# Kernel optimization log

Hardware: AMD Instinct MI355X
Metric: run time of the kernel (lower is better)

Reference implementation:

```python
import jax, jax.numpy as jnp
import numpy as np

D_MODEL = 1024
NUM_HEADS = 16
HEAD_DIM = D_MODEL // NUM_HEADS
B, S = 4, 2048


def setup_inputs() -> dict:
    key = jax.random.key(0)
    ks = jax.random.split(key, 11)
    sc = 1.0 / np.sqrt(D_MODEL)
    return {
        "query": jax.random.normal(ks[0], (B, S, D_MODEL), jnp.float32),
        "key": jax.random.normal(ks[1], (B, S, D_MODEL), jnp.float32),
        "value": jax.random.normal(ks[2], (B, S, D_MODEL), jnp.float32),
        "Wq": jax.random.normal(ks[3], (D_MODEL, D_MODEL), jnp.float32) * sc,
        "bq": jnp.zeros((D_MODEL,), jnp.float32),
        "Wk": jax.random.normal(ks[4], (D_MODEL, D_MODEL), jnp.float32) * sc,
        "bk": jnp.zeros((D_MODEL,), jnp.float32),
        "Wv": jax.random.normal(ks[5], (D_MODEL, D_MODEL), jnp.float32) * sc,
        "bv": jnp.zeros((D_MODEL,), jnp.float32),
        "Wo": jax.random.normal(ks[6], (D_MODEL, D_MODEL), jnp.float32) * sc,
        "bo": jnp.zeros((D_MODEL,), jnp.float32),
    }


def _split_heads(x):
    b, s, _ = x.shape
    return x.reshape(b, s, NUM_HEADS, HEAD_DIM).transpose(0, 2, 1, 3)  # [B,H,S,Dh]


def reference(query, key, value, Wq, bq, Wk, bk, Wv, bv, Wo, bo):
    q = _split_heads(query @ Wq + bq)
    k = _split_heads(key @ Wk + bk)
    v = _split_heads(value @ Wv + bv)
    scores = jnp.einsum("bhqd,bhkd->bhqk", q, k) / np.sqrt(HEAD_DIM)
    attn = jax.nn.softmax(scores, axis=-1)
    out = jnp.einsum("bhqk,bhkd->bhqd", attn, v)
    out = out.transpose(0, 2, 1, 3).reshape(query.shape[0], -1, D_MODEL)
    return out @ Wo + bo
```

## Files before the change

### kernel.cpp

```cpp
#include <hip/hip_runtime.h>

typedef unsigned short u16;
typedef unsigned int   u32;
typedef unsigned long long u64;
typedef __attribute__((ext_vector_type(8))) short bf16x8;
typedef __attribute__((ext_vector_type(4))) float f32x4;

#define S_  2048
#define DH  64
#define DM  1024
#define BS  8192
#define CS  0.18033688011112042f

static __device__ __forceinline__ float bf2f(u16 v){ return __uint_as_float(((u32)v)<<16); }
static __device__ __forceinline__ u16 f2bf(float f){
  u32 x = __float_as_uint(f);
  return (u16)((x + 0x7fffu + ((x>>16)&1u)) >> 16);
}
#if __has_builtin(__builtin_amdgcn_cvt_pk_bf16_f32)
static __device__ __forceinline__ u32 pk2(float x, float y){
  typedef __attribute__((ext_vector_type(2))) __bf16 bf2v;
  union { bf2v v; u32 u; } c; c.v = __builtin_amdgcn_cvt_pk_bf16_f32(x, y); return c.u;
}
#else
static __device__ __forceinline__ u32 pk2(float x, float y){
  return (u32)f2bf(x) | ((u32)f2bf(y) << 16);
}
#endif
#if __has_builtin(__builtin_amdgcn_exp2f)
#define EXP2F(x) __builtin_amdgcn_exp2f(x)
#else
#define EXP2F(x) exp2f(x)
#endif

static __device__ __forceinline__ void dma16(const u16* g, const u16* l){
  __builtin_amdgcn_global_load_lds(
      (const __attribute__((address_space(1))) u32*)(u64)(uintptr_t)g,
      (__attribute__((address_space(3))) u32*)(u32)(u64)(uintptr_t)l, 16, 0, 0);
}

static __device__ __forceinline__ bf16x8 lds_frag(const u16* p){
  union { bf16x8 f; uint2 u[2]; } w;
  w.u[0] = *(const uint2*)(p);
  w.u[1] = *(const uint2*)(p+4);
  return w.f;
}
static __device__ __forceinline__ bf16x8 frag16v(const u16* p){
  union { bf16x8 f; uint4 u; } w;
  w.u = *(const uint4*)p;
  return w.f;
}
static __device__ __forceinline__ void stage16_bf(const u16* __restrict__ g, u16* s){
  uint4 a = *(const uint4*)g;
  uint4 b = *(const uint4*)(g+8);
  *(uint2*)(s+0)  = make_uint2(a.x,a.y);
  *(uint2*)(s+4)  = make_uint2(a.z,a.w);
  *(uint2*)(s+8)  = make_uint2(b.x,b.y);
  *(uint2*)(s+12) = make_uint2(b.z,b.w);
}
static __device__ __forceinline__ void stage16_f32(const float* __restrict__ g, u16* s){
  float4 a0 = ((const float4*)g)[0];
  float4 a1 = ((const float4*)g)[1];
  float4 a2 = ((const float4*)g)[2];
  float4 a3 = ((const float4*)g)[3];
  *(uint2*)(s+0)  = make_uint2(pk2(a0.x,a0.y), pk2(a0.z,a0.w));
  *(uint2*)(s+4)  = make_uint2(pk2(a1.x,a1.y), pk2(a1.z,a1.w));
  *(uint2*)(s+8)  = make_uint2(pk2(a2.x,a2.y), pk2(a2.z,a2.w));
  *(uint2*)(s+12) = make_uint2(pk2(a3.x,a3.y), pk2(a3.z,a3.w));
}

__global__ __launch_bounds__(256) void prep(
    const void* __restrict__ w0, const void* __restrict__ w1,
    const void* __restrict__ w2, const void* __restrict__ w3,
    u16* t0, u16* t1, u16* t2, u16* t3,
    const void* __restrict__ a0, const void* __restrict__ a1,
    const void* __restrict__ a2,
    u16* c0, u16* c1, u16* c2, const int f32f){
  __shared__ u16 tile[32][33];
  int z = blockIdx.z;
  int tid = threadIdx.x;
  bool f32 = f32f != 0;
  if (z < 4){
    const void* in = z==0?w0 : z==1?w1 : z==2?w2 : w3;
    u16* out = z==0?t0 : z==1?t1 : z==2?t2 : t3;
    int tx = tid & 31, ty = tid >> 5;
    int c  = blockIdx.x*32 + tx;
    int r0 = blockIdx.y*32;
    for (int i=ty;i<32;i+=8){
      long off = (long)(r0+i)*DM + c;
      tile[i][tx] = f32 ? f2bf(((const float*)in)[off]) : ((const u16*)in)[off];
    }
    __syncthreads();
    int rr = r0 + tx, cb = blockIdx.x*32;
    for (int i=ty;i<32;i+=8) out[(long)(cb+i)*DM + rr] = tile[tx][i];
  } else {
    if (!f32) return;
    const void* in = z==4?a0 : z==5?a1 : a2;
    u16* out = z==4?c0 : z==5?c1 : c2;
    long lb = (long)blockIdx.y*32 + blockIdx.x;
    long base = (lb*256 + tid)*8;
    #pragma unroll
    for (int it=0; it<4; it++){
      long i = base + (long)it*2097152;
      const float4* p = (const float4*)((const float*)in + i);
      float4 x = p[0], y = p[1];
      *(uint4*)(out + i) = make_uint4(pk2(x.x,x.y), pk2(x.z,x.w), pk2(y.x,y.y), pk2(y.z,y.w));
    }
  }
}

template<int ADMA>
__global__ __launch_bounds__(256) void gemm_qkv(
    const void* __restrict__ A0, const void* __restrict__ A1, const void* __restrict__ A2,
    const u16* __restrict__ W0, const u16* __restrict__ W1, const u16* __restrict__ W2,
    const void* __restrict__ bv0, const void* __restrict__ bv1, const void* __restrict__ bv2,
    u16* C0, u16* C1, u16* C2, const int f32f){
  constexpr int AST = ADMA ? 32 : 36;
  constexpr int NB  = ADMA ? 2 : 1;
  __shared__ __align__(16) u16 As[NB][128*AST];
  __shared__ __align__(16) u16 Bs[NB][128*32];
  int z = blockIdx.z;
  const void* A  = z==0?A0 : z==1?A1 : A2;
  const u16* BT  = z==0?W0 : z==1?W1 : W2;
  const void* bias = z==0?bv0 : z==1?bv1 : bv2;
  u16* C = z==0?C0 : z==1?C1 : C2;
  const bool aF32 = (!ADMA) && (f32f != 0);
  const bool bF32 = (f32f != 0);
  int tid = threadIdx.x;
  int by = blockIdx.x, bx = blockIdx.y;
  int lane = tid & 63, w = tid >> 6;
  int t = lane & 15, q = lane >> 4;
  int wr = w >> 1, wc = w & 1;
  f32x4 acc[4][4];
  #pragma unroll
  for(int i=0;i<4;i++) for(int j=0;j<4;j++) for(int k=0;k<4;k++) acc[i][j][k]=0.f;

  if constexpr (ADMA){
    int sl = (lane & 7) ^ (lane >> 3);
    int srow = ((lane >> 3) << 1) + (sl >> 2);
    const u16* gA = (const u16*)A + ((long)(by*128 + w*32 + srow)*DM + (sl&3)*8);
    const u16* gB = BT            + ((long)(bx*128 + w*32 + srow)*DM + (sl&3)*8);
    const int lb = w*1024;
    int rdo = ((t>>1)<<6) + (((((t&1)<<2) | q) ^ (t>>1)) << 3);
    dma16(gA,         &As[0][lb]);
    dma16(gA + 16*DM, &As[0][lb + 512]);
    dma16(gB,         &Bs[0][lb]);
    dma16(gB + 16*DM, &Bs[0][lb + 512]);
    for (int k0=0; k0<DM; k0+=32){
      int cur = (k0>>5)&1;
      if (k0+32 < DM){
        dma16(gA + k0+32,         &As[cur^1][lb]);
        dma16(gA + k0+32 + 16*DM, &As[cur^1][lb + 512]);
        dma16(gB + k0+32,         &Bs[cur^1][lb]);
        dma16(gB + k0+32 + 16*DM, &Bs[cur^1][lb + 512]);
        asm volatile("s_waitcnt vmcnt(4)" ::: "memory");
      } else {
        asm volatile("s_waitcnt vmcnt(0)" ::: "memory");
      }
      __builtin_amdgcn_s_barrier();
      bf16x8 af[4], bfr[4];
      const u16* Ar = &As[cur][wr*2048 + rdo];
      const u16* Br = &Bs[cur][wc*2048 + rdo];
      #pragma unroll
      for (int rt=0;rt<4;rt++) af[rt]  = frag16v(Ar + rt*512);
      #pragma unroll
      for (int ct=0;ct<4;ct++) bfr[ct] = frag16v(Br + ct*512);
      #pragma unroll
      for (int rt=0;rt<4;rt++)
        #pragma unroll
        for (int ct=0;ct<4;ct++)
          acc[rt][ct] = __builtin_amdgcn_mfma_f32_16x16x32_bf16(af[rt], bfr[ct], acc[rt][ct], 0,0,0);
      __builtin_amdgcn_s_barrier();
    }
  } else {
    const u16* gB = BT + ((long)(bx*128 + w*32 + (lane>>2))*DM + (lane&3)*8);
    long aoff = (long)(by*128 + (tid>>1))*DM + (tid&1)*16;
    const u16* ArdB = &As[0][(wr*64 + t)*AST + q*8];
    const u16* BrdB = &Bs[0][(wc*64 + t)*32  + q*8];
    for (int k0=0; k0<DM; k0+=32){
      dma16(gB + k0,         &Bs[0][w*1024]);
      dma16(gB + 16*DM + k0, &Bs[0][w*1024 + 512]);
      u16* AsW = &As[0][(tid>>1)*36 + (tid&1)*16];
      if (aF32) stage16_f32((const float*)A + aoff + k0, AsW);
      else      stage16_bf ((const u16*)A  + aoff + k0, AsW);
      __syncthreads();
      bf16x8 af[4], bfr[4];
      #pragma unroll
      for (int rt=0;rt<4;rt++) af[rt]  = lds_frag(ArdB + rt*16*AST);
      #pragma unroll
      for (int ct=0;ct<4;ct++) bfr[ct] = lds_frag(BrdB + ct*16*32);
      #pragma unroll
      for (int rt=0;rt<4;rt++)
        #pragma unroll
        for (int ct=0;ct<4;ct++)
          acc[rt][ct] = __builtin_amdgcn_mfma_f32_16x16x32_bf16(af[rt], bfr[ct], acc[rt][ct], 0,0,0);
      __syncthreads();
    }
  }

  float scale = (z==0) ? CS : 1.0f;
  #pragma unroll
  for (int ct=0;ct<4;ct++){
    int col = bx*128 + wc*64 + ct*16 + t;
    float bvv = bF32 ? ((const float*)bias)[col] : bf2f(((const u16*)bias)[col]);
    #pragma unroll
    for (int rt=0;rt<4;rt++){
      int row0 = by*128 + wr*64 + rt*16 + q*4;
      if (z == 2){
        int bb = row0 >> 11, s = row0 & 2047;
        long vbase = (long)bb*2097152 + (long)col*2048
                   + (s & ~63) + ((rt>>1)<<5) + (q<<3) + ((rt&1)<<2);
        u32 lo = pk2(acc[rt][ct][0]+bvv, acc[rt][ct][1]+bvv);
        u32 hi = pk2(acc[rt][ct][2]+bvv, acc[rt][ct][3]+bvv);
        *(uint2*)(C + vbase) = make_uint2(lo,hi);
      } else {
        #pragma unroll
        for (int r=0;r<4;r++)
          C[(long)(row0+r)*DM + col] = f2bf((acc[rt][ct][r] + bvv)*scale);
      }
    }
  }
}

__global__ __launch_bounds__(256) void gemm_o(const u16* __restrict__ A,
    const u16* __restrict__ BT, const void* __restrict__ bias, void* __restrict__ C,
    const int f32f){
  __shared__ __align__(16) u16 As[2][128*32];
  __shared__ __align__(16) u16 Bs[2][128*32];
  const int f = f32f;
  int tid = threadIdx.x;
  int by = blockIdx.x, bx = blockIdx.y;
  int lane = tid & 63, w = tid >> 6;
  int t = lane & 15, q = lane >> 4;
  int wr = w >> 1, wc = w & 1;
  f32x4 acc[4][4];
  #pragma unroll
  for(int i=0;i<4;i++) for(int j=0;j<4;j++) for(int k=0;k<4;k++) acc[i][j][k]=0.f;

  int sl = (lane & 7) ^ (lane >> 3);
  int srow = ((lane >> 3) << 1) + (sl >> 2);
  const u16* gA = A  + ((long)(by*128 + w*32 + srow)*DM + (sl&3)*8);
  const u16* gB = BT + ((long)(bx*128 + w*32 + srow)*DM + (sl&3)*8);
  const int lb = w*1024;
  int rdo = ((t>>1)<<6) + (((((t&1)<<2) | q) ^ (t>>1)) << 3);
  dma16(gA,         &As[0][lb]);
  dma16(gA + 16*DM, &As[0][lb + 512]);
  dma16(gB,         &Bs[0][lb]);
  dma16(gB + 16*DM, &Bs[0][lb + 512]);
  for (int k0=0; k0<DM; k0+=32){
    int cur = (k0>>5)&1;
    if (k0+32 < DM){
      dma16(gA + k0+32,         &As[cur^1][lb]);
      dma16(gA + k0+32 + 16*DM, &As[cur^1][lb + 512]);
      dma16(gB + k0+32,         &Bs[cur^1][lb]);
      dma16(gB + k0+32 + 16*DM, &Bs[cur^1][lb + 512]);
      asm volatile("s_waitcnt vmcnt(4)" ::: "memory");
    } else {
      asm volatile("s_waitcnt vmcnt(0)" ::: "memory");
    }
    __builtin_amdgcn_s_barrier();
    bf16x8 af[4], bfr[4];
    const u16* Ar = &As[cur][wr*2048 + rdo];
    const u16* Br = &Bs[cur][wc*2048 + rdo];
    #pragma unroll
    for (int rt=0;rt<4;rt++) af[rt]  = frag16v(Ar + rt*512);
    #pragma unroll
    for (int ct=0;ct<4;ct++) bfr[ct] = frag16v(Br + ct*512);
    #pragma unroll
    for (int rt=0;rt<4;rt++)
      #pragma unroll
      for (int ct=0;ct<4;ct++)
        acc[rt][ct] = __builtin_amdgcn_mfma_f32_16x16x32_bf16(af[rt], bfr[ct], acc[rt][ct], 0,0,0);
    __builtin_amdgcn_s_barrier();
  }
  #pragma unroll
  for (int ct=0;ct<4;ct++){
    int col = bx*128 + wc*64 + ct*16 + t;
    float bvv = f ? ((const float*)bias)[col] : bf2f(((const u16*)bias)[col]);
    #pragma unroll
    for (int rt=0;rt<4;rt++){
      int row0 = by*128 + wr*64 + rt*16 + q*4;
      #pragma unroll
      for (int r=0;r<4;r++){
        long idx = (long)(row0+r)*DM + col;
        float v = acc[rt][ct][r] + bvv;
        if (f) ((float*)C)[idx] = v;
        else   ((u16*)C)[idx]  = f2bf(v);
      }
    }
  }
}

__global__ __launch_bounds__(256,4) void attn5(const u16* __restrict__ Q,
    const u16* __restrict__ Kb, const u16* __restrict__ Vt, u16* __restrict__ O){
  __shared__ __align__(16) u16 Ks[2][4096];
  __shared__ __align__(16) u16 Vs[2][4096];
  int tid = threadIdx.x;
  int bid = blockIdx.x;
  int qt = bid >> 6;
  int s6 = bid & 63;
  int bh = (s6 & 7)*8 + (s6 >> 3);
  int b = bh >> 4, h = bh & 15;
  int lane = tid & 63, w = tid >> 6;
  int t = lane & 15, q = lane >> 4;

  const u16* Qbase = Q + ((long)(b*S_ + qt*128 + w*32 + t)*DM + h*DH + q*8);
  bf16x8 qf[2][2];
  qf[0][0] = frag16v(Qbase);
  qf[0][1] = frag16v(Qbase + 32);
  qf[1][0] = frag16v(Qbase + 16*DM);
  qf[1][1] = frag16v(Qbase + 16*DM + 32);

  int r0 = tid >> 3;
  int cb = ((tid & 7) * 16) ^ ((r0 & 7) << 4);
  const char* gK = (const char*)Kb + (((long)(b*S_ + r0)*DM + h*DH) << 1) + cb;
  const char* gV = (const char*)Vt + ((((long)bh << 17) + ((long)r0 << 11)) << 1) + cb;
  const long gK1 = ((long)32*DM) << 1;
  const long gV1 = ((long)32*S_) << 1;
  const int ld0 = w*512, ld1 = 2048 + w*512;

  f32x4 o[2][4];
  #pragma unroll
  for (int i=0;i<2;i++) for (int j=0;j<4;j++) for (int k=0;k<4;k++) o[i][j][k]=0.f;
  f32x4 o4[2];
  #pragma unroll
  for (int i=0;i<2;i++) for (int k=0;k<4;k++) o4[i][k]=0.f;

  union { bf16x8 f; u32 u[4]; } vone;
  { u32 ovv = (t==0) ? 0x3F803F80u : 0u;
    vone.u[0]=ovv; vone.u[1]=ovv; vone.u[2]=ovv; vone.u[3]=ovv; }

  const int xorv = (t & 7) << 4;

  dma16((const u16*)(gK),       &Ks[0][ld0]);
  dma16((const u16*)(gK + gK1), &Ks[0][ld1]);
  dma16((const u16*)(gV),       &Vs[0][ld0]);
  dma16((const u16*)(gV + gV1), &Vs[0][ld1]);

  for (int kt=0; kt<32; kt++){
    int cur = kt & 1;
    if (kt < 31){
      long ko = ((long)(kt+1)*64*DM) << 1;
      long vo = (long)(kt+1) << 7;
      dma16((const u16*)(gK + ko),       &Ks[cur^1][ld0]);
      dma16((const u16*)(gK + ko + gK1), &Ks[cur^1][ld1]);
      dma16((const u16*)(gV + vo),       &Vs[cur^1][ld0]);
      dma16((const u16*)(gV + vo + gV1), &Vs[cur^1][ld1]);
      asm volatile("s_waitcnt vmcnt(4)" ::: "memory");
    } else {
      asm volatile("s_waitcnt vmcnt(0)" ::: "memory");
    }
    __builtin_amdgcn_s_barrier();

    const u16* Kc = Ks[cur];
    const u16* Vc = Vs[cur];

    f32x4 sacc[2][4];
    #pragma unroll
    for (int i=0;i<2;i++) for (int j=0;j<4;j++) for (int k=0;k<4;k++) sacc[i][j][k]=0.f;
    #pragma unroll
    for (int ks=0; ks<2; ks++){
      int off = ((ks*64 + q*16) ^ xorv) >> 1;
      bf16x8 k0 = frag16v(Kc + (t     )*64 + off);
      bf16x8 k1 = frag16v(Kc + (16 + t)*64 + off);
      bf16x8 k2 = frag16v(Kc + (32 + t)*64 + off);
      bf16x8 k3 = frag16v(Kc + (48 + t)*64 + off);
      __builtin_amdgcn_s_setprio(1);
      #pragma unroll
      for (int rt=0; rt<2; rt++){
        sacc[rt][0] = __builtin_amdgcn_mfma_f32_16x16x32_bf16(k0, qf[rt][ks], sacc[rt][0],0,0,0);
        sacc[rt][1] = __builtin_amdgcn_mfma_f32_16x16x32_bf16(k1, qf[rt][ks], sacc[rt][1],0,0,0);
        sacc[rt][2] = __builtin_amdgcn_mfma_f32_16x16x32_bf16(k2, qf[rt][ks], sacc[rt][2],0,0,0);
        sacc[rt][3] = __builtin_amdgcn_mfma_f32_16x16x32_bf16(k3, qf[rt][ks], sacc[rt][3],0,0,0);
      }
      __builtin_amdgcn_s_setprio(0);
    }

    union { bf16x8 f; u32 u[4]; } af[2][2];
    #pragma unroll
    for (int rt=0; rt<2; rt++){
      float ev[4][4];
      #pragma unroll
      for (int c=0; c<4; c++)
        #pragma unroll
        for (int r=0; r<4; r++) ev[c][r] = EXP2F(sacc[rt][c][r]);
      #pragma unroll
      for (int ks=0; ks<2; ks++){
        af[rt][ks].u[0] = pk2(ev[2*ks  ][0], ev[2*ks  ][1]);
        af[rt][ks].u[1] = pk2(ev[2*ks  ][2], ev[2*ks  ][3]);
        af[rt][ks].u[2] = pk2(ev[2*ks+1][0], ev[2*ks+1][1]);
        af[rt][ks].u[3] = pk2(ev[2*ks+1][2], ev[2*ks+1][3]);
      }
    }

    #pragma unroll
    for (int ks=0; ks<2; ks++){
      int off = ((ks*64 + q*16) ^ xorv) >> 1;
      bf16x8 v0 = frag16v(Vc + (t     )*64 + off);
      bf16x8 v1 = frag16v(Vc + (16 + t)*64 + off);
      bf16x8 v2 = frag16v(Vc + (32 + t)*64 + off);
      bf16x8 v3 = frag16v(Vc + (48 + t)*64 + off);
      __builtin_amdgcn_s_setprio(1);
      #pragma unroll
      for (int rt=0; rt<2; rt++){
        o[rt][0] = __builtin_amdgcn_mfma_f32_16x16x32_bf16(af[rt][ks].f, v0, o[rt][0],0,0,0);
        o[rt][1] = __builtin_amdgcn_mfma_f32_16x16x32_bf16(af[rt][ks].f, v1, o[rt][1],0,0,0);
        o[rt][2] = __builtin_amdgcn_mfma_f32_16x16x32_bf16(af[rt][ks].f, v2, o[rt][2],0,0,0);
        o[rt][3] = __builtin_amdgcn_mfma_f32_16x16x32_bf16(af[rt][ks].f, v3, o[rt][3],0,0,0);
        o4[rt]   = __builtin_amdgcn_mfma_f32_16x16x32_bf16(af[rt][ks].f, vone.f, o4[rt],0,0,0);
      }
      __builtin_amdgcn_s_setprio(0);
    }
    __builtin_amdgcn_s_barrier();
  }

  #pragma unroll
  for (int rt=0; rt<2; rt++){
    #pragma unroll
    for (int r=0; r<4; r++){
      float l = __shfl(o4[rt][r], lane & 48);
      float inv = 1.f / l;
      int row = qt*128 + w*32 + rt*16 + q*4 + r;
      #pragma unroll
      for (int ct=0; ct<4; ct++)
        O[(long)(b*S_ + row)*DM + h*DH + ct*16 + t] = f2bf(o[rt][ct][r] * inv);
    }
  }
}

extern "C" void kernel_launch(void* const* d_in, const int* in_sizes, int n_in,
                              void* d_out, int out_size, void* d_ws, size_t ws_size,
                              hipStream_t stream){
  (void)n_in; (void)out_size;
  const void* xq = d_in[0];
  const void* xk = d_in[1];
  const void* xv = d_in[2];
  const void* Wq = d_in[3];
  const void* bq = d_in[4];
  const void* Wk = d_in[5];
  const void* bk = d_in[6];
  const void* Wv = d_in[7];
  const void* bv = d_in[8];
  const void* Wo = d_in[9];
  const void* bo = d_in[10];

  const long NT = (long)BS*DM;
  int f32f = 1;
  if (in_sizes && in_sizes[0] == (int)(NT*2)) f32f = 0;

  u16* base = (u16*)((char*)d_ws + 256);
  u16* Qb  = base;
  u16* Kbf = base + NT;
  u16* Vt  = base + 2*NT;
  u16* WqT = base + 3*NT;
  u16* WkT = WqT + (long)DM*DM;
  u16* WvT = WkT + (long)DM*DM;
  u16* WoT = WvT + (long)DM*DM;
  u16* Xc0 = WoT + (long)DM*DM;
  u16* Xc1 = Xc0 + NT;
  u16* Xc2 = Xc1 + NT;
  size_t need_pre = 256 + (size_t)(6*NT + 4*(long)DM*DM)*2;
  bool pre = ws_size >= need_pre;

  dim3 gb(256,1,1);
  int nz = (pre && f32f) ? 7 : 4;
  prep<<<dim3(32,32,nz), gb, 0, stream>>>(Wq, Wk, Wv, Wo,
      WqT, WkT, WvT, WoT, xq, xk, xv, Xc0, Xc1, Xc2, f32f);

  if (pre){
    const void* Aq = f32f ? (const void*)Xc0 : xq;
    const void* Ak = f32f ? (const void*)Xc1 : xk;
    const void* Av = f32f ? (const void*)Xc2 : xv;
    gemm_qkv<1><<<dim3(64,8,3), gb, 0, stream>>>(Aq, Ak, Av,
        WqT, WkT, WvT, bq, bk, bv, Qb, Kbf, Vt, f32f);
  } else {
    gemm_qkv<0><<<dim3(64,8,3), gb, 0, stream>>>(xq, xk, xv,
        WqT, WkT, WvT, bq, bk, bv, Qb, Kbf, Vt, f32f);
  }

  attn5<<<dim3(1024,1,1), gb, 0, stream>>>(Qb, Kbf, Vt, Qb );

  gemm_o<<<dim3(64,8,1), gb, 0, stream>>>(Qb, WoT, bo, d_out, f32f);
}
```

Before: 352.7 us.

## Fuse fp32-to-bf16 activation conversion into QKV GEMM with register-prefetched staging

```diff
diff --git a/kernel.cpp b/kernel.cpp
--- a/kernel.cpp
+++ b/kernel.cpp
@@ -39,92 +39,47 @@
       (__attribute__((address_space(3))) u32*)(u32)(u64)(uintptr_t)l, 16, 0, 0);
 }
 
-static __device__ __forceinline__ bf16x8 lds_frag(const u16* p){
-  union { bf16x8 f; uint2 u[2]; } w;
-  w.u[0] = *(const uint2*)(p);
-  w.u[1] = *(const uint2*)(p+4);
-  return w.f;
-}
 static __device__ __forceinline__ bf16x8 frag16v(const u16* p){
   union { bf16x8 f; uint4 u; } w;
   w.u = *(const uint4*)p;
   return w.f;
 }
-static __device__ __forceinline__ void stage16_bf(const u16* __restrict__ g, u16* s){
-  uint4 a = *(const uint4*)g;
-  uint4 b = *(const uint4*)(g+8);
-  *(uint2*)(s+0)  = make_uint2(a.x,a.y);
-  *(uint2*)(s+4)  = make_uint2(a.z,a.w);
-  *(uint2*)(s+8)  = make_uint2(b.x,b.y);
-  *(uint2*)(s+12) = make_uint2(b.z,b.w);
-}
-static __device__ __forceinline__ void stage16_f32(const float* __restrict__ g, u16* s){
-  float4 a0 = ((const float4*)g)[0];
-  float4 a1 = ((const float4*)g)[1];
-  float4 a2 = ((const float4*)g)[2];
-  float4 a3 = ((const float4*)g)[3];
-  *(uint2*)(s+0)  = make_uint2(pk2(a0.x,a0.y), pk2(a0.z,a0.w));
-  *(uint2*)(s+4)  = make_uint2(pk2(a1.x,a1.y), pk2(a1.z,a1.w));
-  *(uint2*)(s+8)  = make_uint2(pk2(a2.x,a2.y), pk2(a2.z,a2.w));
-  *(uint2*)(s+12) = make_uint2(pk2(a3.x,a3.y), pk2(a3.z,a3.w));
-}
 
 __global__ __launch_bounds__(256) void prep(
     const void* __restrict__ w0, const void* __restrict__ w1,
     const void* __restrict__ w2, const void* __restrict__ w3,
-    u16* t0, u16* t1, u16* t2, u16* t3,
-    const void* __restrict__ a0, const void* __restrict__ a1,
-    const void* __restrict__ a2,
-    u16* c0, u16* c1, u16* c2, const int f32f){
+    u16* t0, u16* t1, u16* t2, u16* t3, const int f32f){
   __shared__ u16 tile[32][33];
   int z = blockIdx.z;
   int tid = threadIdx.x;
   bool f32 = f32f != 0;
-  if (z < 4){
-    const void* in = z==0?w0 : z==1?w1 : z==2?w2 : w3;
-    u16* out = z==0?t0 : z==1?t1 : z==2?t2 : t3;
-    int tx = tid & 31, ty = tid >> 5;
-    int c  = blockIdx.x*32 + tx;
-    int r0 = blockIdx.y*32;
-    for (int i=ty;i<32;i+=8){
-      long off = (long)(r0+i)*DM + c;
-      tile[i][tx] = f32 ? f2bf(((const float*)in)[off]) : ((const u16*)in)[off];
-    }
-    __syncthreads();
-    int rr = r0 + tx, cb = blockIdx.x*32;
-    for (int i=ty;i<32;i+=8) out[(long)(cb+i)*DM + rr] = tile[tx][i];
-  } else {
-    if (!f32) return;
-    const void* in = z==4?a0 : z==5?a1 : a2;
-    u16* out = z==4?c0 : z==5?c1 : c2;
-    long lb = (long)blockIdx.y*32 + blockIdx.x;
-    long base = (lb*256 + tid)*8;
-    #pragma unroll
-    for (int it=0; it<4; it++){
-      long i = base + (long)it*2097152;
-      const float4* p = (const float4*)((const float*)in + i);
-      float4 x = p[0], y = p[1];
-      *(uint4*)(out + i) = make_uint4(pk2(x.x,x.y), pk2(x.z,x.w), pk2(y.x,y.y), pk2(y.z,y.w));
-    }
-  }
-}
-
-template<int ADMA>
+  const void* in = z==0?w0 : z==1?w1 : z==2?w2 : w3;
+  u16* out = z==0?t0 : z==1?t1 : z==2?t2 : t3;
+  int tx = tid & 31, ty = tid >> 5;
+  int c  = blockIdx.x*32 + tx;
+  int r0 = blockIdx.y*32;
+  for (int i=ty;i<32;i+=8){
+    long off = (long)(r0+i)*DM + c;
+    tile[i][tx] = f32 ? f2bf(((const float*)in)[off]) : ((const u16*)in)[off];
+  }
+  __syncthreads();
+  int rr = r0 + tx, cb = blockIdx.x*32;
+  for (int i=ty;i<32;i+=8) out[(long)(cb+i)*DM + rr] = tile[tx][i];
+}
+
+template<int AF32>
 __global__ __launch_bounds__(256) void gemm_qkv(
     const void* __restrict__ A0, const void* __restrict__ A1, const void* __restrict__ A2,
     const u16* __restrict__ W0, const u16* __restrict__ W1, const u16* __restrict__ W2,
     const void* __restrict__ bv0, const void* __restrict__ bv1, const void* __restrict__ bv2,
     u16* C0, u16* C1, u16* C2, const int f32f){
-  constexpr int AST = ADMA ? 32 : 36;
-  constexpr int NB  = ADMA ? 2 : 1;
-  __shared__ __align__(16) u16 As[NB][128*AST];
-  __shared__ __align__(16) u16 Bs[NB][128*32];
+  __shared__ __align__(16) u16 As[2][128*32];
+  __shared__ __align__(16) u16 Bs[2][128*32];
   int z = blockIdx.z;
   const void* A  = z==0?A0 : z==1?A1 : A2;
   const u16* BT  = z==0?W0 : z==1?W1 : W2;
   const void* bias = z==0?bv0 : z==1?bv1 : bv2;
   u16* C = z==0?C0 : z==1?C1 : C2;
-  const bool aF32 = (!ADMA) && (f32f != 0);
   const bool bF32 = (f32f != 0);
   int tid = threadIdx.x;
   int by = blockIdx.x, bx = blockIdx.y;
@@ -135,67 +90,86 @@
   #pragma unroll
   for(int i=0;i<4;i++) for(int j=0;j<4;j++) for(int k=0;k<4;k++) acc[i][j][k]=0.f;
 
-  if constexpr (ADMA){
-    int sl = (lane & 7) ^ (lane >> 3);
-    int srow = ((lane >> 3) << 1) + (sl >> 2);
-    const u16* gA = (const u16*)A + ((long)(by*128 + w*32 + srow)*DM + (sl&3)*8);
-    const u16* gB = BT            + ((long)(bx*128 + w*32 + srow)*DM + (sl&3)*8);
-    const int lb = w*1024;
-    int rdo = ((t>>1)<<6) + (((((t&1)<<2) | q) ^ (t>>1)) << 3);
-    dma16(gA,         &As[0][lb]);
-    dma16(gA + 16*DM, &As[0][lb + 512]);
-    dma16(gB,         &Bs[0][lb]);
-    dma16(gB + 16*DM, &Bs[0][lb + 512]);
-    for (int k0=0; k0<DM; k0+=32){
-      int cur = (k0>>5)&1;
-      if (k0+32 < DM){
-        dma16(gA + k0+32,         &As[cur^1][lb]);
-        dma16(gA + k0+32 + 16*DM, &As[cur^1][lb + 512]);
+  int sl = (lane & 7) ^ (lane >> 3);
+  int srow = ((lane >> 3) << 1) + (sl >> 2);
+  const u16* gB = BT + ((long)(bx*128 + w*32 + srow)*DM + (sl&3)*8);
+  const int lb = w*1024;
+  int rdo = ((t>>1)<<6) + (((((t&1)<<2) | q) ^ (t>>1)) << 3);
+
+  const u16* gA16 = nullptr;
+  const float* gAf = nullptr;
+  u32 woff0 = 0, woff1 = 0;
+  if constexpr (AF32){
+    int arow = lane >> 1;
+    int akk  = (lane & 1) * 16;
+    gAf = (const float*)A + ((long)(by*128 + w*32 + arow)*DM + akk);
+    int line = arow >> 1;
+    int key  = line & 7;
+    int sil0 = ((arow & 1) << 2) | ((lane & 1) << 1);
+    woff0 = lb + line*64 + (u32)(((sil0    ) ^ key) << 3);
+    woff1 = lb + line*64 + (u32)(((sil0 + 1) ^ key) << 3);
+  } else {
+    gA16 = (const u16*)A + ((long)(by*128 + w*32 + srow)*DM + (sl&3)*8);
+  }
+
+  if constexpr (AF32){
+    float4 f0 = ((const float4*)gAf)[0];
+    float4 f1 = ((const float4*)gAf)[1];
+    float4 f2 = ((const float4*)gAf)[2];
+    float4 f3 = ((const float4*)gAf)[3];
+    *(uint4*)(&As[0][woff0]) = make_uint4(pk2(f0.x,f0.y),pk2(f0.z,f0.w),pk2(f1.x,f1.y),pk2(f1.z,f1.w));
+    *(uint4*)(&As[0][woff1]) = make_uint4(pk2(f2.x,f2.y),pk2(f2.z,f2.w),pk2(f3.x,f3.y),pk2(f3.z,f3.w));
+  } else {
+    dma16(gA16,         &As[0][lb]);
+    dma16(gA16 + 16*DM, &As[0][lb + 512]);
+  }
+  dma16(gB,         &Bs[0][lb]);
+  dma16(gB + 16*DM, &Bs[0][lb + 512]);
+
+  for (int k0=0; k0<DM; k0+=32){
+    int cur = (k0>>5)&1;
+    float4 f0, f1, f2, f3;
+    if (k0+32 < DM){
+      if constexpr (AF32){
+        const float* ga = gAf + (k0+32);
+        f0 = ((const float4*)ga)[0];
+        f1 = ((const float4*)ga)[1];
+        f2 = ((const float4*)ga)[2];
+        f3 = ((const float4*)ga)[3];
         dma16(gB + k0+32,         &Bs[cur^1][lb]);
         dma16(gB + k0+32 + 16*DM, &Bs[cur^1][lb + 512]);
+        asm volatile("s_waitcnt vmcnt(6)" ::: "memory");
+      } else {
+        dma16(gA16 + k0+32,         &As[cur^1][lb]);
+        dma16(gA16 + k0+32 + 16*DM, &As[cur^1][lb + 512]);
+        dma16(gB + k0+32,           &Bs[cur^1][lb]);
+        dma16(gB + k0+32 + 16*DM,   &Bs[cur^1][lb + 512]);
         asm volatile("s_waitcnt vmcnt(4)" ::: "memory");
-      } else {
-        asm volatile("s_waitcnt vmcnt(0)" ::: "memory");
-      }
-      __builtin_amdgcn_s_barrier();
-      bf16x8 af[4], bfr[4];
-      const u16* Ar = &As[cur][wr*2048 + rdo];
-      const u16* Br = &Bs[cur][wc*2048 + rdo];
-      #pragma unroll
-      for (int rt=0;rt<4;rt++) af[rt]  = frag16v(Ar + rt*512);
-      #pragma unroll
-      for (int ct=0;ct<4;ct++) bfr[ct] = frag16v(Br + ct*512);
-      #pragma unroll
-      for (int rt=0;rt<4;rt++)
-        #pragma unroll
-        for (int ct=0;ct<4;ct++)
-          acc[rt][ct] = __builtin_amdgcn_mfma_f32_16x16x32_bf16(af[rt], bfr[ct], acc[rt][ct], 0,0,0);
-      __builtin_amdgcn_s_barrier();
-    }
-  } else {
-    const u16* gB = BT + ((long)(bx*128 + w*32 + (lane>>2))*DM + (lane&3)*8);
-    long aoff = (long)(by*128 + (tid>>1))*DM + (tid&1)*16;
-    const u16* ArdB = &As[0][(wr*64 + t)*AST + q*8];
-    const u16* BrdB = &Bs[0][(wc*64 + t)*32  + q*8];
-    for (int k0=0; k0<DM; k0+=32){
-      dma16(gB + k0,         &Bs[0][w*1024]);
-      dma16(gB + 16*DM + k0, &Bs[0][w*1024 + 512]);
-      u16* AsW = &As[0][(tid>>1)*36 + (tid&1)*16];
-      if (aF32) stage16_f32((const float*)A + aoff + k0, AsW);
-      else      stage16_bf ((const u16*)A  + aoff + k0, AsW);
-      __syncthreads();
-      bf16x8 af[4], bfr[4];
-      #pragma unroll
-      for (int rt=0;rt<4;rt++) af[rt]  = lds_frag(ArdB + rt*16*AST);
-      #pragma unroll
-      for (int ct=0;ct<4;ct++) bfr[ct] = lds_frag(BrdB + ct*16*32);
-      #pragma unroll
-      for (int rt=0;rt<4;rt++)
-        #pragma unroll
-        for (int ct=0;ct<4;ct++)
-          acc[rt][ct] = __builtin_amdgcn_mfma_f32_16x16x32_bf16(af[rt], bfr[ct], acc[rt][ct], 0,0,0);
-      __syncthreads();
-    }
+      }
+    } else {
+      asm volatile("s_waitcnt vmcnt(0)" ::: "memory");
+    }
+    asm volatile("s_waitcnt lgkmcnt(0)" ::: "memory");
+    __builtin_amdgcn_s_barrier();
+    bf16x8 af[4], bfr[4];
+    const u16* Ar = &As[cur][wr*2048 + rdo];
+    const u16* Br = &Bs[cur][wc*2048 + rdo];
+    #pragma unroll
+    for (int rt=0;rt<4;rt++) af[rt]  = frag16v(Ar + rt*512);
+    #pragma unroll
+    for (int ct=0;ct<4;ct++) bfr[ct] = frag16v(Br + ct*512);
+    #pragma unroll
+    for (int rt=0;rt<4;rt++)
+      #pragma unroll
+      for (int ct=0;ct<4;ct++)
+        acc[rt][ct] = __builtin_amdgcn_mfma_f32_16x16x32_bf16(af[rt], bfr[ct], acc[rt][ct], 0,0,0);
+    if constexpr (AF32){
+      if (k0+32 < DM){
+        *(uint4*)(&As[cur^1][woff0]) = make_uint4(pk2(f0.x,f0.y),pk2(f0.z,f0.w),pk2(f1.x,f1.y),pk2(f1.z,f1.w));
+        *(uint4*)(&As[cur^1][woff1]) = make_uint4(pk2(f2.x,f2.y),pk2(f2.z,f2.w),pk2(f3.x,f3.y),pk2(f3.z,f3.w));
+      }
+    }
+    __builtin_amdgcn_s_barrier();
   }
 
   float scale = (z==0) ? CS : 1.0f;
@@ -431,7 +405,7 @@
 extern "C" void kernel_launch(void* const* d_in, const int* in_sizes, int n_in,
                               void* d_out, int out_size, void* d_ws, size_t ws_size,
                               hipStream_t stream){
-  (void)n_in; (void)out_size;
+  (void)n_in; (void)out_size; (void)ws_size;
   const void* xq = d_in[0];
   const void* xk = d_in[1];
   const void* xv = d_in[2];
@@ -456,22 +430,13 @@
   u16* WkT = WqT + (long)DM*DM;
   u16* WvT = WkT + (long)DM*DM;
   u16* WoT = WvT + (long)DM*DM;
-  u16* Xc0 = WoT + (long)DM*DM;
-  u16* Xc1 = Xc0 + NT;
-  u16* Xc2 = Xc1 + NT;
-  size_t need_pre = 256 + (size_t)(6*NT + 4*(long)DM*DM)*2;
-  bool pre = ws_size >= need_pre;
 
   dim3 gb(256,1,1);
-  int nz = (pre && f32f) ? 7 : 4;
-  prep<<<dim3(32,32,nz), gb, 0, stream>>>(Wq, Wk, Wv, Wo,
-      WqT, WkT, WvT, WoT, xq, xk, xv, Xc0, Xc1, Xc2, f32f);
-
-  if (pre){
-    const void* Aq = f32f ? (const void*)Xc0 : xq;
-    const void* Ak = f32f ? (const void*)Xc1 : xk;
-    const void* Av = f32f ? (const void*)Xc2 : xv;
-    gemm_qkv<1><<<dim3(64,8,3), gb, 0, stream>>>(Aq, Ak, Av,
+  prep<<<dim3(32,32,4), gb, 0, stream>>>(Wq, Wk, Wv, Wo,
+      WqT, WkT, WvT, WoT, f32f);
+
+  if (f32f){
+    gemm_qkv<1><<<dim3(64,8,3), gb, 0, stream>>>(xq, xk, xv,
         WqT, WkT, WvT, bq, bk, bv, Qb, Kbf, Vt, f32f);
   } else {
     gemm_qkv<0><<<dim3(64,8,3), gb, 0, stream>>>(xq, xk, xv,
```

After: 385.1 us. 9.2% more time.
